# Optimization experiments

Hardware: AMD Instinct MI355X
Metric: run time of the kernel (lower is better)

## Reference

```python
import jax, jax.numpy as jnp
import numpy as np

# physical constants (repo-level globals)
L1, L2, M1, M2 = 1.0, 1.0, 1.0, 1.0
G, K1 = 9.81, 0.5
A_E = 1.0   # energy-shaping stabilizer gain (a_M = 0 -> F_M term is exactly zero)
B_DAMP = 0.0
BATCH, HID = 500000, 64


def _V(q, W1, b1, W2, b2, W3, b3):
    # learned potential: [B,2] -> [B,1]
    h = jnp.tanh(q @ W1 + b1)
    h = jnp.tanh(h @ W2 + b2)
    return h @ W3 + b3


def _pot(q1, q2):
    return -G * (jnp.cos(q1 + q2) * L2 * M2 + jnp.cos(q1) * L1 * (M1 + M2)) + K1 * (0.5 * jnp.pi - q2) ** 2


def _inv_mass(q2):
    M_11 = 2 * jnp.cos(q2) * L1 * L2 * M2 + L2 ** 2 * M2 + L1 ** 2 * (M1 + M2)
    M_12 = L2 * (jnp.cos(q2) * L1 + L2) * M2
    M_22 = L2 ** 2 * M2
    DEN = M_11 * M_22 - M_12 ** 2
    return M_22 / DEN, -M_12 / DEN, M_11 / DEN


def setup_inputs() -> dict:
    key = jax.random.key(0)
    ks = jax.random.split(key, 8)
    s1 = 1.0 / np.sqrt(2.0)
    s2 = 1.0 / np.sqrt(HID)
    return {
        "x": jax.random.normal(ks[0], (BATCH, 4), jnp.float32),
        "t": jnp.zeros((1,), jnp.float32),
        "W1": jax.random.normal(ks[1], (2, HID), jnp.float32) * s1,
        "b1": jnp.zeros((HID,), jnp.float32),
        "W2": jax.random.normal(ks[2], (HID, HID), jnp.float32) * s2,
        "b2": jnp.zeros((HID,), jnp.float32),
        "W3": jax.random.normal(ks[3], (HID, 1), jnp.float32) * s2,
        "b3": jnp.zeros((1,), jnp.float32),
        "T_param": jnp.ones((1,), jnp.float32),
        "x0": jax.random.normal(ks[4], (4,), jnp.float32),
    }


def _forward(x, W1, b1, W2, b2, W3, b3, T_param, x0):
    q = x[:, :2]
    p = x[:, 2:]
    q1, q2 = q[:, 0], q[:, 1]
    p1, p2 = p[:, 0], p[:, 1]

    # u_energy_shaping = -dV/dq
    dVdq = jax.grad(lambda qq: _V(qq, W1, b1, W2, b2, W3, b3).sum())(q)
    u_es = -dVdq  # [B,2]

    # stabilizing control (a_M = 0 -> only F_E term)
    iM11, iM12, iM22 = _inv_mass(q2)
    quad = iM11 * p1 ** 2 + 2 * iM12 * p1 * p2 + iM22 * p2 ** 2  # p^T M^{-1} p
    kin = 0.5 * quad
    E = _pot(q1, q2) + kin + _V(q, W1, b1, W2, b2, W3, b3)[:, 0]

    # desired energy from x0 (set in _set_control_parameters)
    q0 = x0[:2][None, :]
    p0 = x0[2:]
    i011, i012, i022 = _inv_mass(q0[:, 1])
    kin0 = 0.5 * (i011 * p0[0] ** 2 + 2 * i012 * p0[0] * p0[1] + i022 * p0[1] ** 2)
    E_des = (_pot(q0[:, 0], q0[:, 1]) + kin0 + _V(q0, W1, b1, W2, b2, W3, b3)[:, 0])[0]

    pnorm = jnp.sqrt(quad)
    safe = jnp.where(pnorm > 0, pnorm, 1.0)
    p_hat = jnp.where((pnorm > 0)[:, None], p / safe[:, None], p)
    u_st = A_E * (E_des - E)[:, None] * p_hat

    u = u_es + u_st
    u1, u2 = u[:, 0], u[:, 1]

    # dynamics
    cq2, sq2 = jnp.cos(q2), jnp.sin(q2)
    DET = L1 ** 2 * L2 ** 2 * M2 ** 2 * (-(cq2 ** 2)) + L1 ** 2 * L2 ** 2 * M2 ** 2 + L1 ** 2 * L2 ** 2 * M1 * M2
    dq1dt = L2 ** 2 * M2 * p1 / DET - L2 * M2 * p2 * (L1 * cq2 + L2) / DET
    dq2dt = p2 * (2 * L2 * L1 * M2 * cq2 + L1 ** 2 * (M1 + M2) + L2 ** 2 * M2) / DET - L2 * M2 * p1 * (L1 * cq2 + L2) / DET
    dp1dt = -G * (jnp.sin(q1 + q2) * L2 * M2 + jnp.sin(q1) * L1 * (M1 + M2)) + u1 - B_DAMP * dq1dt
    denom = L1 ** 2 * L2 ** 2 * (M1 + sq2 ** 2 * M2) ** 2
    inner = (-(p2 ** 2) * sq2 * (cq2 * L1 + L2) * (cq2 * L2 * M2 + L1 * (M1 + M2))
             + 0.5 * p1 * p2 * sq2 * L2 * (4 * cq2 * L2 * M2 + L1 * (2 * M1 + (3 + jnp.cos(2 * q2)) * M2))
             + L2 ** 2 * (-cq2 * p1 ** 2 * sq2 * M2
                          + L1 ** 2 * (M1 + sq2 ** 2 * M2) ** 2 * (G * jnp.sin(q1 + q2) * L2 * M2 - K1 * (jnp.pi - 2 * q2))))
    dp2dt = -(inner / denom) + u2 - B_DAMP * dq2dt

    dxdt = jnp.stack([dq1dt, dq2dt, dp1dt, dp2dt], axis=1)
    return jnp.abs(T_param[0]) * dxdt


def reference(x, t, W1, b1, W2, b2, W3, b3, T_param, x0):
    # t is unused by the forward math (autonomous dynamics under ODE-solver interface)
    return _forward(x, W1, b1, W2, b2, W3, b3, T_param, x0)
```

## Files before the change

kernel.cpp:

```cpp
#include <hip/hip_runtime.h>
#include <math.h>

#define HID 64

typedef __attribute__((ext_vector_type(4))) float f32x4;
typedef __attribute__((ext_vector_type(8))) __bf16 bf16x8;
typedef __attribute__((ext_vector_type(4))) __bf16 bf16x4;

__device__ __forceinline__ float fast_tanh(float x) {
    float e = __expf(2.0f * x);
    return 1.0f - 2.0f * __builtin_amdgcn_rcpf(e + 1.0f);
}

__global__ void prep_kernel(const float* __restrict__ W1, const float* __restrict__ b1,
                            const float* __restrict__ W2, const float* __restrict__ b2,
                            const float* __restrict__ W3, const float* __restrict__ b3,
                            const float* __restrict__ x0, float* __restrict__ edes_out,
                            __bf16* __restrict__ W2bf, __bf16* __restrict__ W2Tbf) {
    int tid = threadIdx.x;
    for (int idx = tid; idx < HID * HID; idx += 256) {
        W2bf[idx] = (__bf16)W2[idx];
        int r = idx >> 6, c = idx & 63;
        W2Tbf[idx] = (__bf16)W2[c * HID + r];
    }
    if (tid < 64) {
        int j = tid;
        float q1 = x0[0], q2 = x0[1], p1 = x0[2], p2 = x0[3];
        float h1j = fast_tanh(fmaf(q1, W1[j], fmaf(q2, W1[HID + j], b1[j])));
        float z = b2[j];
#pragma unroll 1
        for (int i = 0; i < HID; i++) {
            float hi = __shfl(h1j, i, 64);
            z = fmaf(hi, W2[i * HID + j], z);
        }
        float h2 = fast_tanh(z);
        float v = h2 * W3[j];
#pragma unroll
        for (int off = 32; off; off >>= 1) v += __shfl_xor(v, off, 64);
        if (j == 0) {
            float V = v + b3[0];
            float s, c;
            __sincosf(q2, &s, &c);
            float DEN = 2.0f - c * c;
            float rDEN = __builtin_amdgcn_rcpf(DEN);
            float quad = (p1 * p1 - 2.0f * (c + 1.0f) * p1 * p2 + (2.0f * c + 3.0f) * p2 * p2) * rDEN;
            float kin = 0.5f * quad;
            float s1, c1;
            __sincosf(q1, &s1, &c1);
            float c12 = c1 * c - s1 * s;
            float dq = 1.57079632679489662f - q2;
            float pot = -9.81f * (c12 + 2.0f * c1) + 0.5f * dq * dq;
            edes_out[0] = pot + kin + V;
        }
    }
}

#define TANH8(F, Q1v, Q2v)                                                  \
    F[0] = (__bf16)fast_tanh(fmaf(Q1v, wa0.x, fmaf(Q2v, wb0.x, bb0.x)));    \
    F[1] = (__bf16)fast_tanh(fmaf(Q1v, wa0.y, fmaf(Q2v, wb0.y, bb0.y)));    \
    F[2] = (__bf16)fast_tanh(fmaf(Q1v, wa0.z, fmaf(Q2v, wb0.z, bb0.z)));    \
    F[3] = (__bf16)fast_tanh(fmaf(Q1v, wa0.w, fmaf(Q2v, wb0.w, bb0.w)));    \
    F[4] = (__bf16)fast_tanh(fmaf(Q1v, wa1.x, fmaf(Q2v, wb1.x, bb1.x)));    \
    F[5] = (__bf16)fast_tanh(fmaf(Q1v, wa1.y, fmaf(Q2v, wb1.y, bb1.y)));    \
    F[6] = (__bf16)fast_tanh(fmaf(Q1v, wa1.z, fmaf(Q2v, wb1.z, bb1.z)));    \
    F[7] = (__bf16)fast_tanh(fmaf(Q1v, wa1.w, fmaf(Q2v, wb1.w, bb1.w)));

#define L1HALF4(FA, FB, FC, FD, K0)                                         \
    do {                                                                    \
        const float4 wa0 = *(const float4*)(W1 + (K0));                     \
        const float4 wa1 = *(const float4*)(W1 + (K0) + 4);                 \
        const float4 wb0 = *(const float4*)(W1 + HID + (K0));               \
        const float4 wb1 = *(const float4*)(W1 + HID + (K0) + 4);           \
        const float4 bb0 = *(const float4*)(b1 + (K0));                     \
        const float4 bb1 = *(const float4*)(b1 + (K0) + 4);                 \
        TANH8(FA, q1A, q2A)                                                 \
        TANH8(FB, q1B, q2B)                                                 \
        TANH8(FC, q1C, q2C)                                                 \
        TANH8(FD, q1D, q2D)                                                 \
    } while (0)

#define MFMA __builtin_amdgcn_mfma_f32_16x16x32_bf16

#define G1MT(MT, ZA, ZB, ZC, ZD)                                            \
    do {                                                                    \
        const bf16x8 wf0 = *(const bf16x8*)(w2t + (MT) * 1024);             \
        ZA = MFMA(wf0, a10A, ZA, 0, 0, 0);                                  \
        ZB = MFMA(wf0, a10B, ZB, 0, 0, 0);                                  \
        ZC = MFMA(wf0, a10C, ZC, 0, 0, 0);                                  \
        ZD = MFMA(wf0, a10D, ZD, 0, 0, 0);                                  \
        const bf16x8 wf1 = *(const bf16x8*)(w2t + (MT) * 1024 + 32);        \
        ZA = MFMA(wf1, a11A, ZA, 0, 0, 0);                                  \
        ZB = MFMA(wf1, a11B, ZB, 0, 0, 0);                                  \
        ZC = MFMA(wf1, a11C, ZC, 0, 0, 0);                                  \
        ZD = MFMA(wf1, a11D, ZD, 0, 0, 0);                                  \
    } while (0)

#define H2ONE(Z, VP, GBUF, MT)                                                      \
    do {                                                                            \
        float h, g0_, g1_, g2_, g3_;                                                \
        h = fast_tanh(Z[0]); VP = fmaf(h, w3v.x, VP); g0_ = w3v.x * (1.0f - h * h); \
        h = fast_tanh(Z[1]); VP = fmaf(h, w3v.y, VP); g1_ = w3v.y * (1.0f - h * h); \
        h = fast_tanh(Z[2]); VP = fmaf(h, w3v.z, VP); g2_ = w3v.z * (1.0f - h * h); \
        h = fast_tanh(Z[3]); VP = fmaf(h, w3v.w, VP); g3_ = w3v.w * (1.0f - h * h); \
        bf16x4 gv = {(__bf16)g0_, (__bf16)g1_, (__bf16)g2_, (__bf16)g3_};           \
        *(bf16x4*)((GBUF) + rowbase + ((16 * (MT) + 4 * hi) ^ swz)) = gv;           \
    } while (0)

#define H2MT4(MT, ZA, ZB, ZC, ZD)                                           \
    do {                                                                    \
        const float4 w3v = *(const float4*)(W3 + 16 * (MT) + 4 * hi);       \
        H2ONE(ZA, vpA, g2A, MT);                                            \
        H2ONE(ZB, vpB, g2B, MT);                                            \
        H2ONE(ZC, vpC, g2C, MT);                                            \
        H2ONE(ZD, vpD, g2D, MT);                                            \
    } while (0)

#define G2MT(MT, RA, RB, RC, RD)                                            \
    do {                                                                    \
        const bf16x8 wf0 = *(const bf16x8*)(w2b + (MT) * 1024);             \
        RA = MFMA(wf0, a20A, RA, 0, 0, 0);                                  \
        RB = MFMA(wf0, a20B, RB, 0, 0, 0);                                  \
        RC = MFMA(wf0, a20C, RC, 0, 0, 0);                                  \
        RD = MFMA(wf0, a20D, RD, 0, 0, 0);                                  \
        const bf16x8 wf1 = *(const bf16x8*)(w2b + (MT) * 1024 + 32);        \
        RA = MFMA(wf1, a21A, RA, 0, 0, 0);                                  \
        RB = MFMA(wf1, a21B, RB, 0, 0, 0);                                  \
        RC = MFMA(wf1, a21C, RC, 0, 0, 0);                                  \
        RD = MFMA(wf1, a21D, RD, 0, 0, 0);                                  \
    } while (0)

#define DVONE(R, Q1v, Q2v, D1, D2)                                                            \
    do {                                                                                      \
        float hf, gi;                                                                         \
        hf = fast_tanh(fmaf(Q1v, w1av.x, fmaf(Q2v, w1bv.x, b1v.x)));                          \
        gi = (1.0f - hf * hf) * R[0]; D1 = fmaf(w1av.x, gi, D1); D2 = fmaf(w1bv.x, gi, D2);   \
        hf = fast_tanh(fmaf(Q1v, w1av.y, fmaf(Q2v, w1bv.y, b1v.y)));                          \
        gi = (1.0f - hf * hf) * R[1]; D1 = fmaf(w1av.y, gi, D1); D2 = fmaf(w1bv.y, gi, D2);   \
        hf = fast_tanh(fmaf(Q1v, w1av.z, fmaf(Q2v, w1bv.z, b1v.z)));                          \
        gi = (1.0f - hf * hf) * R[2]; D1 = fmaf(w1av.z, gi, D1); D2 = fmaf(w1bv.z, gi, D2);   \
        hf = fast_tanh(fmaf(Q1v, w1av.w, fmaf(Q2v, w1bv.w, b1v.w)));                          \
        gi = (1.0f - hf * hf) * R[3]; D1 = fmaf(w1av.w, gi, D1); D2 = fmaf(w1bv.w, gi, D2);   \
    } while (0)

#define DVMT4(MT, RA, RB, RC, RD)                                           \
    do {                                                                    \
        const float4 w1av = *(const float4*)(W1 + 16 * (MT) + 4 * hi);      \
        const float4 w1bv = *(const float4*)(W1 + HID + 16 * (MT) + 4 * hi);\
        const float4 b1v  = *(const float4*)(b1 + 16 * (MT) + 4 * hi);      \
        DVONE(RA, q1A, q2A, d1A, d2A);                                      \
        DVONE(RB, q1B, q2B, d1B, d2B);                                      \
        DVONE(RC, q1C, q2C, d1C, d2C);                                      \
        DVONE(RD, q1D, q2D, d1D, d2D);                                      \
    } while (0)

#define RED2(V) V += __shfl_xor(V, 16, 64); V += __shfl_xor(V, 32, 64);

#define SEL4(A, B, C, D) ((hi == 0) ? (A) : (hi == 1) ? (B) : (hi == 2) ? (C) : (D))

__global__ __launch_bounds__(256, 3) void pend_kernel(
    const float4* __restrict__ x,
    const float* __restrict__ W1, const float* __restrict__ b1,
    const __bf16* __restrict__ W2bf, const __bf16* __restrict__ W2Tbf,
    const float* __restrict__ b2,
    const float* __restrict__ W3, const float* __restrict__ b3,
    const float* __restrict__ Tp, const float* __restrict__ edes_p,
    float4* __restrict__ out, int n)
{
    __shared__ __align__(16) __bf16 lds[4 * 4096];
    const int tid = threadIdx.x;
    const int w = tid >> 6, l = tid & 63;
    const int lo = l & 15, hi = l >> 4;
    __bf16* g2A = lds + w * 4096;
    __bf16* g2B = g2A + 1024;
    __bf16* g2C = g2B + 1024;
    __bf16* g2D = g2C + 1024;

    const float E_des = edes_p[0];
    const float Tabs = fabsf(Tp[0]);
    const float b3c = b3[0];

    const int base = blockIdx.x * 256 + w * 64;
    int eA = base + lo;       if (eA >= n) eA = n - 1;
    int eB = base + 16 + lo;  if (eB >= n) eB = n - 1;
    int eC = base + 32 + lo;  if (eC >= n) eC = n - 1;
    int eD = base + 48 + lo;  if (eD >= n) eD = n - 1;
    const float4 xvA = x[eA];
    const float4 xvB = x[eB];
    const float4 xvC = x[eC];
    const float4 xvD = x[eD];
    const float q1A = xvA.x, q2A = xvA.y, p1A = xvA.z, p2A = xvA.w;
    const float q1B = xvB.x, q2B = xvB.y, p1B = xvB.z, p2B = xvB.w;
    const float q1C = xvC.x, q2C = xvC.y, p1C = xvC.z, p2C = xvC.w;
    const float q1D = xvD.x, q2D = xvD.y, p1D = xvD.z, p2D = xvD.w;

    const int swz = (lo & 7) << 3;
    const int rowbase = lo * HID;

    bf16x8 a10A, a11A, a10B, a11B, a10C, a11C, a10D, a11D;
    L1HALF4(a10A, a10B, a10C, a10D, 8 * hi);
    L1HALF4(a11A, a11B, a11C, a11D, 32 + 8 * hi);

    const __bf16* w2t = W2Tbf + lo * HID + 8 * hi;
    const __bf16* w2b = W2bf  + lo * HID + 8 * hi;

    const float4 b2v0 = *(const float4*)(b2 + 4 * hi);
    const float4 b2v1 = *(const float4*)(b2 + 16 + 4 * hi);
    const float4 b2v2 = *(const float4*)(b2 + 32 + 4 * hi);
    const float4 b2v3 = *(const float4*)(b2 + 48 + 4 * hi);
    f32x4 zA0 = {b2v0.x, b2v0.y, b2v0.z, b2v0.w};
    f32x4 zA1 = {b2v1.x, b2v1.y, b2v1.z, b2v1.w};
    f32x4 zA2 = {b2v2.x, b2v2.y, b2v2.z, b2v2.w};
    f32x4 zA3 = {b2v3.x, b2v3.y, b2v3.z, b2v3.w};
    f32x4 zB0 = zA0, zB1 = zA1, zB2 = zA2, zB3 = zA3;
    f32x4 zC0 = zA0, zC1 = zA1, zC2 = zA2, zC3 = zA3;
    f32x4 zD0 = zA0, zD1 = zA1, zD2 = zA2, zD3 = zA3;
    G1MT(0, zA0, zB0, zC0, zD0);
    G1MT(1, zA1, zB1, zC1, zD1);
    G1MT(2, zA2, zB2, zC2, zD2);
    G1MT(3, zA3, zB3, zC3, zD3);

    float vpA = 0.0f, vpB = 0.0f, vpC = 0.0f, vpD = 0.0f;
    H2MT4(0, zA0, zB0, zC0, zD0);
    H2MT4(1, zA1, zB1, zC1, zD1);
    H2MT4(2, zA2, zB2, zC2, zD2);
    H2MT4(3, zA3, zB3, zC3, zD3);

    const bf16x8 a20A = *(const bf16x8*)(g2A + rowbase + ((8 * hi) ^ swz));
    const bf16x8 a21A = *(const bf16x8*)(g2A + rowbase + ((32 + 8 * hi) ^ swz));
    const bf16x8 a20B = *(const bf16x8*)(g2B + rowbase + ((8 * hi) ^ swz));
    const bf16x8 a21B = *(const bf16x8*)(g2B + rowbase + ((32 + 8 * hi) ^ swz));
    const bf16x8 a20C = *(const bf16x8*)(g2C + rowbase + ((8 * hi) ^ swz));
    const bf16x8 a21C = *(const bf16x8*)(g2C + rowbase + ((32 + 8 * hi) ^ swz));
    const bf16x8 a20D = *(const bf16x8*)(g2D + rowbase + ((8 * hi) ^ swz));
    const bf16x8 a21D = *(const bf16x8*)(g2D + rowbase + ((32 + 8 * hi) ^ swz));
    f32x4 rA0 = {0.f, 0.f, 0.f, 0.f}, rA1 = rA0, rA2 = rA0, rA3 = rA0;
    f32x4 rB0 = rA0, rB1 = rA0, rB2 = rA0, rB3 = rA0;
    f32x4 rC0 = rA0, rC1 = rA0, rC2 = rA0, rC3 = rA0;
    f32x4 rD0 = rA0, rD1 = rA0, rD2 = rA0, rD3 = rA0;
    G2MT(0, rA0, rB0, rC0, rD0);
    G2MT(1, rA1, rB1, rC1, rD1);
    G2MT(2, rA2, rB2, rC2, rD2);
    G2MT(3, rA3, rB3, rC3, rD3);

    float d1A = 0.f, d2A = 0.f, d1B = 0.f, d2B = 0.f;
    float d1C = 0.f, d2C = 0.f, d1D = 0.f, d2D = 0.f;
    DVMT4(0, rA0, rB0, rC0, rD0);
    DVMT4(1, rA1, rB1, rC1, rD1);
    DVMT4(2, rA2, rB2, rC2, rD2);
    DVMT4(3, rA3, rB3, rC3, rD3);

    RED2(vpA) RED2(vpB) RED2(vpC) RED2(vpD)
    RED2(d1A) RED2(d1B) RED2(d1C) RED2(d1D)
    RED2(d2A) RED2(d2B) RED2(d2C) RED2(d2D)

    const float V    = SEL4(vpA, vpB, vpC, vpD) + b3c;
    const float dVq1 = SEL4(d1A, d1B, d1C, d1D);
    const float dVq2 = SEL4(d2A, d2B, d2C, d2D);
    const float q1 = SEL4(q1A, q1B, q1C, q1D);
    const float q2 = SEL4(q2A, q2B, q2C, q2D);
    const float p1 = SEL4(p1A, p1B, p1C, p1D);
    const float p2 = SEL4(p2A, p2B, p2C, p2D);

    float s2q, c2q, s1q, c1q;
    __sincosf(q2, &s2q, &c2q);
    __sincosf(q1, &s1q, &c1q);
    const float s12 = s1q * c2q + c1q * s2q;
    const float c12 = c1q * c2q - s1q * s2q;

    const float cc = c2q, s = s2q;
    const float DEN = 2.0f - cc * cc;
    const float rDEN = __builtin_amdgcn_rcpf(DEN);
    const float cp1 = cc + 1.0f;

    const float quad = (p1 * p1 - 2.0f * cp1 * p1 * p2 + (2.0f * cc + 3.0f) * p2 * p2) * rDEN;
    const float kin = 0.5f * quad;
    const float dqa = 1.57079632679489662f - q2;
    const float pot = -9.81f * (c12 + 2.0f * c1q) + 0.5f * dqa * dqa;
    const float E = pot + kin + V;

    const float fac = (quad > 0.0f) ? __builtin_amdgcn_rsqf(quad) : 1.0f;
    const float coef = E_des - E;
    const float u1 = -dVq1 + coef * p1 * fac;
    const float u2 = -dVq2 + coef * p2 * fac;

    const float dq1dt = (p1 - cp1 * p2) * rDEN;
    const float dq2dt = ((2.0f * cc + 3.0f) * p2 - cp1 * p1) * rDEN;
    const float dp1dt = -9.81f * (s12 + 2.0f * s1q) + u1;

    const float inner = -p2 * p2 * s * cp1 * (cc + 2.0f)
                + p1 * p2 * s * (fmaf(cc, cc, fmaf(2.0f, cc, 2.0f)))
                - cc * p1 * p1 * s
                + DEN * DEN * (fmaf(9.81f, s12, -0.5f * (3.14159265358979324f - 2.0f * q2)));
    const float dp2dt = -(inner * rDEN * rDEN) + u2;

    const int row = base + l;
    if (row < n) {
        float4 o;
        o.x = Tabs * dq1dt;
        o.y = Tabs * dq2dt;
        o.z = Tabs * dp1dt;
        o.w = Tabs * dp2dt;
        out[row] = o;
    }
}

extern "C" void kernel_launch(void* const* d_in, const int* in_sizes, int n_in,
                              void* d_out, int out_size, void* d_ws, size_t ws_size,
                              hipStream_t stream) {
    const float* x  = (const float*)d_in[0];
    const float* W1 = (const float*)d_in[2];
    const float* b1 = (const float*)d_in[3];
    const float* W2 = (const float*)d_in[4];
    const float* b2 = (const float*)d_in[5];
    const float* W3 = (const float*)d_in[6];
    const float* b3 = (const float*)d_in[7];
    const float* Tp = (const float*)d_in[8];
    const float* x0 = (const float*)d_in[9];

    float* ws = (float*)d_ws;
    float* edes = ws;
    __bf16* W2bf  = (__bf16*)(ws + 16);
    __bf16* W2Tbf = W2bf + HID * HID;

    prep_kernel<<<1, 256, 0, stream>>>(W1, b1, W2, b2, W3, b3, x0, edes, W2bf, W2Tbf);

    int n = in_sizes[0] / 4;
    int blocks = (n + 255) / 256;
    pend_kernel<<<blocks, 256, 0, stream>>>((const float4*)x, W1, b1, W2bf, W2Tbf,
                                            b2, W3, b3, Tp, edes, (float4*)d_out, n);
}
```

Before: 51.49 us.

## Interleave MFMA and tanh epilogue per tile to cut live accumulators, raise occupancy

Fuses each layer-2 MFMA M-tile with its tanh/derivative epilogue, and likewise each backward MFMA tile with its dV accumulation, so only four f32x4 accumulators are live at a time instead of sixteen. This lowers register pressure, and the launch bound is raised from 3 to 4 waves-per-EU minimum accordingly. The risk is less independent MFMA work available to hide latency behind transcendental math, unless the compiler re-schedules across tiles, and possible spills if the new register cap is too tight.

```diff
diff --git a/kernel.cpp b/kernel.cpp
--- a/kernel.cpp
+++ b/kernel.cpp
@@ -81,20 +81,6 @@
 
 #define MFMA __builtin_amdgcn_mfma_f32_16x16x32_bf16
 
-#define G1MT(MT, ZA, ZB, ZC, ZD)                                            \
-    do {                                                                    \
-        const bf16x8 wf0 = *(const bf16x8*)(w2t + (MT) * 1024);             \
-        ZA = MFMA(wf0, a10A, ZA, 0, 0, 0);                                  \
-        ZB = MFMA(wf0, a10B, ZB, 0, 0, 0);                                  \
-        ZC = MFMA(wf0, a10C, ZC, 0, 0, 0);                                  \
-        ZD = MFMA(wf0, a10D, ZD, 0, 0, 0);                                  \
-        const bf16x8 wf1 = *(const bf16x8*)(w2t + (MT) * 1024 + 32);        \
-        ZA = MFMA(wf1, a11A, ZA, 0, 0, 0);                                  \
-        ZB = MFMA(wf1, a11B, ZB, 0, 0, 0);                                  \
-        ZC = MFMA(wf1, a11C, ZC, 0, 0, 0);                                  \
-        ZD = MFMA(wf1, a11D, ZD, 0, 0, 0);                                  \
-    } while (0)
-
 #define H2ONE(Z, VP, GBUF, MT)                                                      \
     do {                                                                            \
         float h, g0_, g1_, g2_, g3_;                                                \
@@ -106,27 +92,26 @@
         *(bf16x4*)((GBUF) + rowbase + ((16 * (MT) + 4 * hi) ^ swz)) = gv;           \
     } while (0)
 
-#define H2MT4(MT, ZA, ZB, ZC, ZD)                                           \
+#define FWDMT(MT)                                                           \
     do {                                                                    \
+        const float4 b2v = *(const float4*)(b2 + 16 * (MT) + 4 * hi);       \
+        f32x4 zA = {b2v.x, b2v.y, b2v.z, b2v.w};                            \
+        f32x4 zB = zA, zC = zA, zD = zA;                                    \
+        const bf16x8 wf0 = *(const bf16x8*)(w2t + (MT) * 1024);             \
+        zA = MFMA(wf0, a10A, zA, 0, 0, 0);                                  \
+        zB = MFMA(wf0, a10B, zB, 0, 0, 0);                                  \
+        zC = MFMA(wf0, a10C, zC, 0, 0, 0);                                  \
+        zD = MFMA(wf0, a10D, zD, 0, 0, 0);                                  \
+        const bf16x8 wf1 = *(const bf16x8*)(w2t + (MT) * 1024 + 32);        \
+        zA = MFMA(wf1, a11A, zA, 0, 0, 0);                                  \
+        zB = MFMA(wf1, a11B, zB, 0, 0, 0);                                  \
+        zC = MFMA(wf1, a11C, zC, 0, 0, 0);                                  \
+        zD = MFMA(wf1, a11D, zD, 0, 0, 0);                                  \
         const float4 w3v = *(const float4*)(W3 + 16 * (MT) + 4 * hi);       \
-        H2ONE(ZA, vpA, g2A, MT);                                            \
-        H2ONE(ZB, vpB, g2B, MT);                                            \
-        H2ONE(ZC, vpC, g2C, MT);                                            \
-        H2ONE(ZD, vpD, g2D, MT);                                            \
-    } while (0)
-
-#define G2MT(MT, RA, RB, RC, RD)                                            \
-    do {                                                                    \
-        const bf16x8 wf0 = *(const bf16x8*)(w2b + (MT) * 1024);             \
-        RA = MFMA(wf0, a20A, RA, 0, 0, 0);                                  \
-        RB = MFMA(wf0, a20B, RB, 0, 0, 0);                                  \
-        RC = MFMA(wf0, a20C, RC, 0, 0, 0);                                  \
-        RD = MFMA(wf0, a20D, RD, 0, 0, 0);                                  \
-        const bf16x8 wf1 = *(const bf16x8*)(w2b + (MT) * 1024 + 32);        \
-        RA = MFMA(wf1, a21A, RA, 0, 0, 0);                                  \
-        RB = MFMA(wf1, a21B, RB, 0, 0, 0);                                  \
-        RC = MFMA(wf1, a21C, RC, 0, 0, 0);                                  \
-        RD = MFMA(wf1, a21D, RD, 0, 0, 0);                                  \
+        H2ONE(zA, vpA, g2A, MT);                                            \
+        H2ONE(zB, vpB, g2B, MT);                                            \
+        H2ONE(zC, vpC, g2C, MT);                                            \
+        H2ONE(zD, vpD, g2D, MT);                                            \
     } while (0)
 
 #define DVONE(R, Q1v, Q2v, D1, D2)                                                            \
@@ -142,22 +127,34 @@
         gi = (1.0f - hf * hf) * R[3]; D1 = fmaf(w1av.w, gi, D1); D2 = fmaf(w1bv.w, gi, D2);   \
     } while (0)
 
-#define DVMT4(MT, RA, RB, RC, RD)                                           \
+#define BWDMT(MT)                                                           \
     do {                                                                    \
+        f32x4 rA = {0.f, 0.f, 0.f, 0.f};                                    \
+        f32x4 rB = rA, rC = rA, rD = rA;                                    \
+        const bf16x8 wf0 = *(const bf16x8*)(w2b + (MT) * 1024);             \
+        rA = MFMA(wf0, a20A, rA, 0, 0, 0);                                  \
+        rB = MFMA(wf0, a20B, rB, 0, 0, 0);                                  \
+        rC = MFMA(wf0, a20C, rC, 0, 0, 0);                                  \
+        rD = MFMA(wf0, a20D, rD, 0, 0, 0);                                  \
+        const bf16x8 wf1 = *(const bf16x8*)(w2b + (MT) * 1024 + 32);        \
+        rA = MFMA(wf1, a21A, rA, 0, 0, 0);                                  \
+        rB = MFMA(wf1, a21B, rB, 0, 0, 0);                                  \
+        rC = MFMA(wf1, a21C, rC, 0, 0, 0);                                  \
+        rD = MFMA(wf1, a21D, rD, 0, 0, 0);                                  \
         const float4 w1av = *(const float4*)(W1 + 16 * (MT) + 4 * hi);      \
         const float4 w1bv = *(const float4*)(W1 + HID + 16 * (MT) + 4 * hi);\
         const float4 b1v  = *(const float4*)(b1 + 16 * (MT) + 4 * hi);      \
-        DVONE(RA, q1A, q2A, d1A, d2A);                                      \
-        DVONE(RB, q1B, q2B, d1B, d2B);                                      \
-        DVONE(RC, q1C, q2C, d1C, d2C);                                      \
-        DVONE(RD, q1D, q2D, d1D, d2D);                                      \
+        DVONE(rA, q1A, q2A, d1A, d2A);                                      \
+        DVONE(rB, q1B, q2B, d1B, d2B);                                      \
+        DVONE(rC, q1C, q2C, d1C, d2C);                                      \
+        DVONE(rD, q1D, q2D, d1D, d2D);                                      \
     } while (0)
 
 #define RED2(V) V += __shfl_xor(V, 16, 64); V += __shfl_xor(V, 32, 64);
 
 #define SEL4(A, B, C, D) ((hi == 0) ? (A) : (hi == 1) ? (B) : (hi == 2) ? (C) : (D))
 
-__global__ __launch_bounds__(256, 3) void pend_kernel(
+__global__ __launch_bounds__(256, 4) void pend_kernel(
     const float4* __restrict__ x,
     const float* __restrict__ W1, const float* __restrict__ b1,
     const __bf16* __restrict__ W2bf, const __bf16* __restrict__ W2Tbf,
@@ -203,27 +200,11 @@
     const __bf16* w2t = W2Tbf + lo * HID + 8 * hi;
     const __bf16* w2b = W2bf  + lo * HID + 8 * hi;
 
-    const float4 b2v0 = *(const float4*)(b2 + 4 * hi);
-    const float4 b2v1 = *(const float4*)(b2 + 16 + 4 * hi);
-    const float4 b2v2 = *(const float4*)(b2 + 32 + 4 * hi);
-    const float4 b2v3 = *(const float4*)(b2 + 48 + 4 * hi);
-    f32x4 zA0 = {b2v0.x, b2v0.y, b2v0.z, b2v0.w};
-    f32x4 zA1 = {b2v1.x, b2v1.y, b2v1.z, b2v1.w};
-    f32x4 zA2 = {b2v2.x, b2v2.y, b2v2.z, b2v2.w};
-    f32x4 zA3 = {b2v3.x, b2v3.y, b2v3.z, b2v3.w};
-    f32x4 zB0 = zA0, zB1 = zA1, zB2 = zA2, zB3 = zA3;
-    f32x4 zC0 = zA0, zC1 = zA1, zC2 = zA2, zC3 = zA3;
-    f32x4 zD0 = zA0, zD1 = zA1, zD2 = zA2, zD3 = zA3;
-    G1MT(0, zA0, zB0, zC0, zD0);
-    G1MT(1, zA1, zB1, zC1, zD1);
-    G1MT(2, zA2, zB2, zC2, zD2);
-    G1MT(3, zA3, zB3, zC3, zD3);
-
     float vpA = 0.0f, vpB = 0.0f, vpC = 0.0f, vpD = 0.0f;
-    H2MT4(0, zA0, zB0, zC0, zD0);
-    H2MT4(1, zA1, zB1, zC1, zD1);
-    H2MT4(2, zA2, zB2, zC2, zD2);
-    H2MT4(3, zA3, zB3, zC3, zD3);
+    FWDMT(0);
+    FWDMT(1);
+    FWDMT(2);
+    FWDMT(3);
 
     const bf16x8 a20A = *(const bf16x8*)(g2A + rowbase + ((8 * hi) ^ swz));
     const bf16x8 a21A = *(const bf16x8*)(g2A + rowbase + ((32 + 8 * hi) ^ swz));
@@ -233,21 +214,13 @@
     const bf16x8 a21C = *(const bf16x8*)(g2C + rowbase + ((32 + 8 * hi) ^ swz));
     const bf16x8 a20D = *(const bf16x8*)(g2D + rowbase + ((8 * hi) ^ swz));
     const bf16x8 a21D = *(const bf16x8*)(g2D + rowbase + ((32 + 8 * hi) ^ swz));
-    f32x4 rA0 = {0.f, 0.f, 0.f, 0.f}, rA1 = rA0, rA2 = rA0, rA3 = rA0;
-    f32x4 rB0 = rA0, rB1 = rA0, rB2 = rA0, rB3 = rA0;
-    f32x4 rC0 = rA0, rC1 = rA0, rC2 = rA0, rC3 = rA0;
-    f32x4 rD0 = rA0, rD1 = rA0, rD2 = rA0, rD3 = rA0;
-    G2MT(0, rA0, rB0, rC0, rD0);
-    G2MT(1, rA1, rB1, rC1, rD1);
-    G2MT(2, rA2, rB2, rC2, rD2);
-    G2MT(3, rA3, rB3, rC3, rD3);
 
     float d1A = 0.f, d2A = 0.f, d1B = 0.f, d2B = 0.f;
     float d1C = 0.f, d2C = 0.f, d1D = 0.f, d2D = 0.f;
-    DVMT4(0, rA0, rB0, rC0, rD0);
-    DVMT4(1, rA1, rB1, rC1, rD1);
-    DVMT4(2, rA2, rB2, rC2, rD2);
-    DVMT4(3, rA3, rB3, rC3, rD3);
+    BWDMT(0);
+    BWDMT(1);
+    BWDMT(2);
+    BWDMT(3);
 
     RED2(vpA) RED2(vpB) RED2(vpC) RED2(vpD)
     RED2(d1A) RED2(d1B) RED2(d1C) RED2(d1D)
```

Result: faster. 49.11 us (-4.6%).
